# Performance work log

Hardware: AMD Instinct MI355X
Metric: run time of the kernel (lower is better)

The kernel has to match this reference:

```python
import jax, jax.numpy as jnp
import numpy as np

B, L, D, V, U = 4096, 50, 64, 100000, 256
E = 2 * D          # concat of two seq-feature embeddings
CAT = 3 * E        # concat([q, k, q*k])


def setup_inputs() -> dict:
    key = jax.random.key(0)
    ks = jax.random.split(key, 12)
    inp = {
        "query_ids_item": jax.random.randint(ks[0], (B, 1), 0, V),
        "query_ids_cate": jax.random.randint(ks[1], (B, 1), 0, V),
        "seq_ids_item": jax.random.randint(ks[2], (B, 1, L), 0, V),
        "seq_ids_cate": jax.random.randint(ks[3], (B, 1, L), 0, V),
        "mask": jax.random.randint(ks[4], (B, 1, L), 0, 2).astype(bool),
        # learned params
        "emb_item": jax.random.normal(ks[5], (V, D), jnp.float32) * 0.05,
        "emb_cate": jax.random.normal(ks[6], (V, D), jnp.float32) * 0.05,
        "W_hide": jax.random.normal(ks[7], (CAT, U), jnp.float32) * (1.0 / np.sqrt(CAT)),
        "b_hide": jnp.zeros((U,), jnp.float32),
        "W_out": jax.random.normal(ks[8], (U, 1), jnp.float32) * (1.0 / np.sqrt(U)),
        "b_out": jnp.zeros((1,), jnp.float32),
    }
    return inp


def reference(query_ids_item, query_ids_cate, seq_ids_item, seq_ids_cate, mask,
              emb_item, emb_cate, W_hide, b_hide, W_out, b_out):
    # Embedding gathers (StdOneHot per seq feature, concat over features)
    q = jnp.concatenate([emb_item[query_ids_item], emb_cate[query_ids_cate]], axis=-1)   # [B,1,E]
    k = jnp.concatenate([emb_item[seq_ids_item], emb_cate[seq_ids_cate]], axis=-1)        # [B,1,L,E]

    # DinAttention: tile query over L, concat([q, k, q*k])
    qt = jnp.broadcast_to(q[:, :, None, :], k.shape)                                       # [B,1,L,E]
    cat = jnp.concatenate([qt, k, qt * k], axis=-1)                                        # [B,1,L,3E]

    h = jax.nn.relu(jnp.einsum('bglc,cu->bglu', cat, W_hide) + b_hide)                     # [B,1,L,U]
    scores = jnp.einsum('bglu,uo->bglo', h, W_out) + b_out                                 # [B,1,L,1]
    scores = jnp.swapaxes(scores, -1, -2)                                                  # [B,1,1,L]

    # mask [B,1,L] -> expand_dims axis=1 -> [B,1,1,L]; multiply (no softmax)
    scores = scores * mask.astype(jnp.float32)[:, None, :, :].reshape(mask.shape[0], 1, 1, -1)

    out = jnp.einsum('bgol,bgle->bgoe', scores, k)                                         # [B,1,1,E]
    return jnp.squeeze(out, axis=-2)                                                       # [B,1,E]
```

## Files before the change

### kernel.cpp

```cpp
#include <hip/hip_runtime.h>
#include <hip/hip_bf16.h>


#define L_SEQ 50
#define LP    64
#define D_EMB 64
#define E_DIM 128
#define U_DIM 256
#define CATK  384
#define V_SZ  100000
#define B_TOT 4096
#define KSTR  136

typedef __bf16 bf16x2 __attribute__((ext_vector_type(2)));
typedef __bf16 bf16x4 __attribute__((ext_vector_type(4)));
typedef __bf16 bf16x8 __attribute__((ext_vector_type(8)));
typedef float  f32x4  __attribute__((ext_vector_type(4)));

__device__ __bf16 g_W3[12288 * 8];

__global__ __launch_bounds__(256) void prep_kernel(const float* __restrict__ W_hide) {
  const int o = blockIdx.x * 256 + threadIdx.x;
  const int s = o >> 10, ut = (o >> 6) & 15, lane = o & 63;
  const int quad = lane >> 4, m = lane & 15;
  const int u = ut * 16 + m;
  const int c0 = s * 32 + quad * 8;
  bf16x8 v;
#pragma unroll
  for (int j = 0; j < 8; ++j)
    v[j] = (__bf16)W_hide[(c0 + j) * 256 + u];
  *(bf16x8*)&g_W3[o * 8] = v;
}

__global__ __launch_bounds__(256, 4) void din_main_kernel(
    const int* __restrict__ qid_item, const int* __restrict__ qid_cate,
    const int* __restrict__ seq_item, const int* __restrict__ seq_cate,
    const int* __restrict__ mask,
    const float* __restrict__ emb_item,
    const float* __restrict__ emb_cate,
    const float* __restrict__ b_hide,
    const float* __restrict__ W_out,
    const float* __restrict__ b_out,
    float* __restrict__ out) {
  __shared__ alignas(16) __bf16 KbA2[2 * LP * KSTR];
  __shared__ alignas(16) float qrowf[E_DIM];
  __shared__ alignas(16) float qv_s[U_DIM];
  __shared__ float mask_f[LP];
  __shared__ float scpart[4][LP];
  __shared__ float scores_s[LP];
  __shared__ float outp[4][E_DIM];
  __bf16* const Kb = KbA2;
  __bf16* const A2 = KbA2 + LP * KSTR;

  const int b = blockIdx.x;
  const int t = threadIdx.x;
  const int r = t >> 2, q4 = t & 3;
  const int col0 = q4 * 32;
  const int wave = t >> 6, lane = t & 63;
  const int m = lane & 15, quad = lane >> 4;

  float4 kv[8];
  if (r < L_SEQ) {
    int id = (q4 < 2) ? seq_item[b * L_SEQ + r] : seq_cate[b * L_SEQ + r];
    if ((unsigned)id >= (unsigned)V_SZ) id = 0;
    const float4* s4 = (const float4*)(((q4 < 2) ? emb_item : emb_cate)
                                       + (size_t)id * D_EMB + (q4 & 1) * 32);
#pragma unroll
    for (int i = 0; i < 8; ++i) kv[i] = s4[i];
  } else {
#pragma unroll
    for (int i = 0; i < 8; ++i) kv[i] = make_float4(0.f, 0.f, 0.f, 0.f);
  }
#pragma unroll
  for (int i = 0; i < 8; ++i) {
    bf16x4 h4 = {(__bf16)kv[i].x, (__bf16)kv[i].y, (__bf16)kv[i].z, (__bf16)kv[i].w};
    *(bf16x4*)&Kb[r * KSTR + col0 + i * 4] = h4;
  }
  if (t < 4) {
    int id = (t < 2) ? qid_item[b] : qid_cate[b];
    if ((unsigned)id >= (unsigned)V_SZ) id = 0;
    const float4* s4 = (const float4*)(((t < 2) ? emb_item : emb_cate)
                                       + (size_t)id * D_EMB + (t & 1) * 32);
    float4* d4 = (float4*)&qrowf[t * 32];
#pragma unroll
    for (int i = 0; i < 8; ++i) d4[i] = s4[i];
  }
  if (t < LP) mask_f[t] = (t < L_SEQ && mask[b * L_SEQ + t] != 0) ? 1.0f : 0.0f;
  __syncthreads();

#pragma unroll
  for (int i = 0; i < 8; ++i) {
    const float* qp = &qrowf[col0 + i * 4];
    bf16x4 h4 = {(__bf16)(kv[i].x * qp[0]), (__bf16)(kv[i].y * qp[1]),
                 (__bf16)(kv[i].z * qp[2]), (__bf16)(kv[i].w * qp[3])};
    *(bf16x4*)&A2[r * KSTR + col0 + i * 4] = h4;
  }
  if (r == 50) {
#pragma unroll
    for (int i = 0; i < 8; ++i) {
      const float* qp = &qrowf[col0 + i * 4];
      bf16x4 h4 = {(__bf16)qp[0], (__bf16)qp[1], (__bf16)qp[2], (__bf16)qp[3]};
      *(bf16x4*)&Kb[50 * KSTR + col0 + i * 4] = h4;
    }
  }
  __syncthreads();

  {
    f32x4 acc2[4];
#pragma unroll
    for (int mt = 0; mt < 4; ++mt) acc2[mt] = (f32x4){0.f, 0.f, 0.f, 0.f};
#pragma unroll
    for (int s = 0; s < 4; ++s) {
      const int klocal = s * 32 + quad * 8;
      bf16x8 kq = *(const bf16x8*)&KbA2[(50 + m) * KSTR + klocal];
      bf16x8 wq[4];
#pragma unroll
      for (int mt = 0; mt < 4; ++mt)
        wq[mt] = *(const bf16x8*)&g_W3[(s * 1024 + (wave * 4 + mt) * 64 + lane) * 8];
#pragma unroll
      for (int mt = 0; mt < 4; ++mt)
        acc2[mt] = __builtin_amdgcn_mfma_f32_16x16x32_bf16(wq[mt], kq, acc2[mt],
                                                           0, 0, 0);
    }
    if (m == 0) {
#pragma unroll
      for (int mt = 0; mt < 4; ++mt) {
        const int u0 = wave * 64 + mt * 16 + quad * 4;
        float4 bh = *(const float4*)&b_hide[u0];
        f32x4 v = acc2[mt];
        v[0] += bh.x; v[1] += bh.y; v[2] += bh.z; v[3] += bh.w;
        *(f32x4*)&qv_s[u0] = v;
      }
    }
  }
  __syncthreads();

  f32x4 acc[4][4];
#pragma unroll
  for (int mt = 0; mt < 4; ++mt)
#pragma unroll
    for (int nt = 0; nt < 4; ++nt) acc[mt][nt] = (f32x4){0.f, 0.f, 0.f, 0.f};

#pragma unroll
  for (int s = 0; s < 8; ++s) {
    const __bf16* Bb = (s < 4) ? Kb : A2;
    const int klocal = (s & 3) * 32 + quad * 8;
    bf16x8 wfr[4], kfr[4];
#pragma unroll
    for (int mt = 0; mt < 4; ++mt) {
      const int o = (4 + s) * 1024 + (wave * 4 + mt) * 64 + lane;
      wfr[mt] = *(const bf16x8*)&g_W3[o * 8];
    }
#pragma unroll
    for (int nt = 0; nt < 4; ++nt)
      kfr[nt] = *(const bf16x8*)&Bb[(nt * 16 + m) * KSTR + klocal];
#pragma unroll
    for (int mt = 0; mt < 4; ++mt)
#pragma unroll
      for (int nt = 0; nt < 4; ++nt)
        acc[mt][nt] = __builtin_amdgcn_mfma_f32_16x16x32_bf16(
            wfr[mt], kfr[nt], acc[mt][nt], 0, 0, 0);
  }

  float qv4[4][4], wo4[4][4];
#pragma unroll
  for (int mt = 0; mt < 4; ++mt) {
    const int u0 = wave * 64 + mt * 16 + quad * 4;
    f32x4 qq = *(const f32x4*)&qv_s[u0];
    float4 ww = *(const float4*)&W_out[u0];
    qv4[mt][0] = qq[0]; qv4[mt][1] = qq[1]; qv4[mt][2] = qq[2]; qv4[mt][3] = qq[3];
    wo4[mt][0] = ww.x;  wo4[mt][1] = ww.y;  wo4[mt][2] = ww.z;  wo4[mt][3] = ww.w;
  }
  float part[4];
#pragma unroll
  for (int nt = 0; nt < 4; ++nt) {
    float sum = 0.f;
#pragma unroll
    for (int mt = 0; mt < 4; ++mt)
#pragma unroll
      for (int rg = 0; rg < 4; ++rg) {
        float h = acc[mt][nt][rg] + qv4[mt][rg];
        h = fmaxf(h, 0.f);
        sum += h * wo4[mt][rg];
      }
    part[nt] = sum;
  }
#pragma unroll
  for (int nt = 0; nt < 4; ++nt) {
    part[nt] += __shfl_xor(part[nt], 16, 64);
    part[nt] += __shfl_xor(part[nt], 32, 64);
  }
  if (lane < 16) {
#pragma unroll
    for (int nt = 0; nt < 4; ++nt)
      scpart[wave][nt * 16 + lane] = part[nt];
  }
  __syncthreads();

  if (t < LP) {
    float s = scpart[0][t] + scpart[1][t] + scpart[2][t] + scpart[3][t]
            + b_out[0];
    scores_s[t] = s * mask_f[t];
  }
  __syncthreads();
  {
    const int e2 = lane * 2;
    float o0 = 0.f, o1 = 0.f;
#pragma unroll
    for (int i = 0; i < 16; ++i) {
      const int l = wave * 16 + i;
      const float sc = scores_s[l];
      bf16x2 kk = *(const bf16x2*)&Kb[l * KSTR + e2];
      o0 += sc * (float)kk[0];
      o1 += sc * (float)kk[1];
    }
    outp[wave][e2]     = o0;
    outp[wave][e2 + 1] = o1;
  }
  __syncthreads();
  if (t < E_DIM) {
    float o = outp[0][t] + outp[1][t] + outp[2][t] + outp[3][t];
    out[(size_t)b * E_DIM + t] = o;
  }
}

extern "C" void kernel_launch(void* const* d_in, const int* in_sizes, int n_in,
                              void* d_out, int out_size, void* d_ws, size_t ws_size,
                              hipStream_t stream) {
  const int* qid_item = (const int*)d_in[0];
  const int* qid_cate = (const int*)d_in[1];
  const int* seq_item = (const int*)d_in[2];
  const int* seq_cate = (const int*)d_in[3];
  const int* mask     = (const int*)d_in[4];
  const float* emb_item = (const float*)d_in[5];
  const float* emb_cate = (const float*)d_in[6];
  const float* W_hide   = (const float*)d_in[7];
  const float* b_hide   = (const float*)d_in[8];
  const float* W_out    = (const float*)d_in[9];
  const float* b_out    = (const float*)d_in[10];
  float* out = (float*)d_out;

  (void)d_ws; (void)ws_size;

  prep_kernel<<<48, 256, 0, stream>>>(W_hide);
  din_main_kernel<<<B_TOT, 256, 0, stream>>>(qid_item, qid_cate, seq_item,
                                             seq_cate, mask, emb_item, emb_cate,
                                             b_hide, W_out, b_out, out);
}
```

Before: 156.3 us.

## Load query row per thread and keep query projection in registers, dropping two barriers

Every thread now loads its slice of the query embedding directly into registers, so the q*k product is formed in the same pass as the key staging. The separate q-row pass and its barrier go away. The query projection MFMA now reads a broadcast bf16 q row and keeps its accumulators in registers, so each lane adds b_hide itself and the qv_s shared buffer and its barrier are removed. The cost is redundant global loads of the query row and more register pressure from the qf array and the accq accumulators, which could lower occupancy.

```diff
diff --git a/kernel.cpp b/kernel.cpp
--- a/kernel.cpp
+++ b/kernel.cpp
@@ -7,7 +7,6 @@
 #define D_EMB 64
 #define E_DIM 128
 #define U_DIM 256
-#define CATK  384
 #define V_SZ  100000
 #define B_TOT 4096
 #define KSTR  136
@@ -42,15 +41,13 @@
     const float* __restrict__ W_out,
     const float* __restrict__ b_out,
     float* __restrict__ out) {
-  __shared__ alignas(16) __bf16 KbA2[2 * LP * KSTR];
-  __shared__ alignas(16) float qrowf[E_DIM];
-  __shared__ alignas(16) float qv_s[U_DIM];
+  __shared__ alignas(16) __bf16 Kb[LP * KSTR];
+  __shared__ alignas(16) __bf16 A2[LP * KSTR];
+  __shared__ alignas(16) __bf16 qrow_h[E_DIM];
   __shared__ float mask_f[LP];
   __shared__ float scpart[4][LP];
   __shared__ float scores_s[LP];
   __shared__ float outp[4][E_DIM];
-  __bf16* const Kb = KbA2;
-  __bf16* const A2 = KbA2 + LP * KSTR;
 
   const int b = blockIdx.x;
   const int t = threadIdx.x;
@@ -59,6 +56,14 @@
   const int wave = t >> 6, lane = t & 63;
   const int m = lane & 15, quad = lane >> 4;
 
+  int qidv = (q4 < 2) ? qid_item[b] : qid_cate[b];
+  if ((unsigned)qidv >= (unsigned)V_SZ) qidv = 0;
+  const float4* qsrc = (const float4*)(((q4 < 2) ? emb_item : emb_cate)
+                                       + (size_t)qidv * D_EMB + (q4 & 1) * 32);
+  float4 qf[8];
+#pragma unroll
+  for (int i = 0; i < 8; ++i) qf[i] = qsrc[i];
+
   float4 kv[8];
   if (r < L_SEQ) {
     int id = (q4 < 2) ? seq_item[b * L_SEQ + r] : seq_cate[b * L_SEQ + r];
@@ -75,65 +80,36 @@
   for (int i = 0; i < 8; ++i) {
     bf16x4 h4 = {(__bf16)kv[i].x, (__bf16)kv[i].y, (__bf16)kv[i].z, (__bf16)kv[i].w};
     *(bf16x4*)&Kb[r * KSTR + col0 + i * 4] = h4;
-  }
-  if (t < 4) {
-    int id = (t < 2) ? qid_item[b] : qid_cate[b];
-    if ((unsigned)id >= (unsigned)V_SZ) id = 0;
-    const float4* s4 = (const float4*)(((t < 2) ? emb_item : emb_cate)
-                                       + (size_t)id * D_EMB + (t & 1) * 32);
-    float4* d4 = (float4*)&qrowf[t * 32];
-#pragma unroll
-    for (int i = 0; i < 8; ++i) d4[i] = s4[i];
+    bf16x4 a4 = {(__bf16)(kv[i].x * qf[i].x), (__bf16)(kv[i].y * qf[i].y),
+                 (__bf16)(kv[i].z * qf[i].z), (__bf16)(kv[i].w * qf[i].w)};
+    *(bf16x4*)&A2[r * KSTR + col0 + i * 4] = a4;
+  }
+  if (r == 0) {
+#pragma unroll
+    for (int i = 0; i < 8; ++i) {
+      bf16x4 h4 = {(__bf16)qf[i].x, (__bf16)qf[i].y, (__bf16)qf[i].z, (__bf16)qf[i].w};
+      *(bf16x4*)&qrow_h[col0 + i * 4] = h4;
+    }
   }
   if (t < LP) mask_f[t] = (t < L_SEQ && mask[b * L_SEQ + t] != 0) ? 1.0f : 0.0f;
   __syncthreads();
 
-#pragma unroll
-  for (int i = 0; i < 8; ++i) {
-    const float* qp = &qrowf[col0 + i * 4];
-    bf16x4 h4 = {(__bf16)(kv[i].x * qp[0]), (__bf16)(kv[i].y * qp[1]),
-                 (__bf16)(kv[i].z * qp[2]), (__bf16)(kv[i].w * qp[3])};
-    *(bf16x4*)&A2[r * KSTR + col0 + i * 4] = h4;
-  }
-  if (r == 50) {
-#pragma unroll
-    for (int i = 0; i < 8; ++i) {
-      const float* qp = &qrowf[col0 + i * 4];
-      bf16x4 h4 = {(__bf16)qp[0], (__bf16)qp[1], (__bf16)qp[2], (__bf16)qp[3]};
-      *(bf16x4*)&Kb[50 * KSTR + col0 + i * 4] = h4;
-    }
-  }
-  __syncthreads();
-
-  {
-    f32x4 acc2[4];
-#pragma unroll
-    for (int mt = 0; mt < 4; ++mt) acc2[mt] = (f32x4){0.f, 0.f, 0.f, 0.f};
-#pragma unroll
-    for (int s = 0; s < 4; ++s) {
-      const int klocal = s * 32 + quad * 8;
-      bf16x8 kq = *(const bf16x8*)&KbA2[(50 + m) * KSTR + klocal];
-      bf16x8 wq[4];
-#pragma unroll
-      for (int mt = 0; mt < 4; ++mt)
-        wq[mt] = *(const bf16x8*)&g_W3[(s * 1024 + (wave * 4 + mt) * 64 + lane) * 8];
-#pragma unroll
-      for (int mt = 0; mt < 4; ++mt)
-        acc2[mt] = __builtin_amdgcn_mfma_f32_16x16x32_bf16(wq[mt], kq, acc2[mt],
-                                                           0, 0, 0);
-    }
-    if (m == 0) {
-#pragma unroll
-      for (int mt = 0; mt < 4; ++mt) {
-        const int u0 = wave * 64 + mt * 16 + quad * 4;
-        float4 bh = *(const float4*)&b_hide[u0];
-        f32x4 v = acc2[mt];
-        v[0] += bh.x; v[1] += bh.y; v[2] += bh.z; v[3] += bh.w;
-        *(f32x4*)&qv_s[u0] = v;
-      }
-    }
-  }
-  __syncthreads();
+  f32x4 accq[4];
+#pragma unroll
+  for (int mt = 0; mt < 4; ++mt) accq[mt] = (f32x4){0.f, 0.f, 0.f, 0.f};
+#pragma unroll
+  for (int s = 0; s < 4; ++s) {
+    const int klocal = s * 32 + quad * 8;
+    bf16x8 kq = *(const bf16x8*)&qrow_h[klocal];
+    bf16x8 wq[4];
+#pragma unroll
+    for (int mt = 0; mt < 4; ++mt)
+      wq[mt] = *(const bf16x8*)&g_W3[(s * 1024 + (wave * 4 + mt) * 64 + lane) * 8];
+#pragma unroll
+    for (int mt = 0; mt < 4; ++mt)
+      accq[mt] = __builtin_amdgcn_mfma_f32_16x16x32_bf16(wq[mt], kq, accq[mt],
+                                                         0, 0, 0);
+  }
 
   f32x4 acc[4][4];
 #pragma unroll
@@ -166,9 +142,10 @@
 #pragma unroll
   for (int mt = 0; mt < 4; ++mt) {
     const int u0 = wave * 64 + mt * 16 + quad * 4;
-    f32x4 qq = *(const f32x4*)&qv_s[u0];
+    float4 bh = *(const float4*)&b_hide[u0];
     float4 ww = *(const float4*)&W_out[u0];
-    qv4[mt][0] = qq[0]; qv4[mt][1] = qq[1]; qv4[mt][2] = qq[2]; qv4[mt][3] = qq[3];
+    qv4[mt][0] = accq[mt][0] + bh.x; qv4[mt][1] = accq[mt][1] + bh.y;
+    qv4[mt][2] = accq[mt][2] + bh.z; qv4[mt][3] = accq[mt][3] + bh.w;
     wo4[mt][0] = ww.x;  wo4[mt][1] = ww.y;  wo4[mt][2] = ww.z;  wo4[mt][3] = ww.w;
   }
   float part[4];
```

New measurement: 169.7 us. +8.5%, slower.
